# Performance work log

Hardware: AMD Instinct MI355X
Metric: run time of the kernel (lower is better)

Reference implementation:

```python
import jax, jax.numpy as jnp
import numpy as np
import math

B, T, N_EMBD = 8, 4096, 512
DIM = 64  # dim_q == dim_k == dim_v


def setup_inputs() -> dict:
    key = jax.random.key(0)
    k1, k2, k3, k4 = jax.random.split(key, 4)
    x = jax.random.normal(k1, (B, T, N_EMBD), dtype=jnp.float32)
    # store Linear weights as [in, out] so projection is x @ W
    w_q = jax.random.normal(k2, (N_EMBD, DIM), dtype=jnp.float32) * 0.02
    w_k = jax.random.normal(k3, (N_EMBD, DIM), dtype=jnp.float32) * 0.02
    w_v = jax.random.normal(k4, (N_EMBD, DIM), dtype=jnp.float32) * 0.02
    return {"x": x, "w_q": w_q, "w_k": w_k, "w_v": w_v}


def reference(x, w_q, w_k, w_v):
    # Faithful to original torch code, INCLUDING the bug v = w_k(x).
    q = jnp.einsum('btn,nd->btd', x, w_q)
    k = jnp.einsum('btn,nd->btd', x, w_k)
    v = jnp.einsum('btn,nd->btd', x, w_k)  # original uses w_k for v (bug preserved)
    scores = jnp.einsum('bqd,bkd->bqk', q, k) / math.sqrt(DIM)  # [B,T,T]
    causal = jnp.tril(jnp.ones((T, T), dtype=bool))
    scores = jnp.where(causal, scores, jnp.float32(-jnp.inf))
    attn = jax.nn.softmax(scores, axis=-1)
    out = jnp.einsum('bqk,bkd->bqd', attn, v)
    return out
```

## Files before the change

kernel.cpp:

```cpp
#include <hip/hip_runtime.h>
#include <math.h>

#define BB 8
#define TT 4096
#define NE 512
#define DD 64

using f32x4 = __attribute__((ext_vector_type(4))) float;
using s16x8 = __attribute__((ext_vector_type(8))) short;

#define EXP2 __builtin_amdgcn_exp2f

__device__ __forceinline__ ushort f2bf(float f) {
  uint u = __builtin_bit_cast(uint, f);
  u += 0x7fffu + ((u >> 16) & 1u);
  return (ushort)(u >> 16);
}
__device__ __forceinline__ uint cvtpk(float lo, float hi) {
  uint r;
  asm("v_cvt_pk_bf16_f32 %0, %1, %2" : "=v"(r) : "v"(lo), "v"(hi));
  return r;
}

#define KTSWZ(d) ((((d) ^ ((d) >> 3)) & 7) << 4)

__global__ __launch_bounds__(256) void prep_kernel(
    const float* __restrict__ wq, const float* __restrict__ wk,
    ushort* __restrict__ WT) {
  const int i = blockIdx.x * 256 + threadIdx.x;
  const int col = i & 127, k = i >> 7;
  const float v = (col < DD) ? wq[(size_t)k * DD + col] * 0.18033688f
                             : wk[(size_t)k * DD + (col - DD)];
  WT[(size_t)col * NE + k] = f2bf(v);
}

__global__ __launch_bounds__(256) void proj_kernel(
    const float* __restrict__ x, const ushort* __restrict__ WT,
    ushort* __restrict__ Qo, ushort* __restrict__ Ko) {
  __shared__ __align__(16) char smem[24576];
  char* As = smem;
  char* Bs = smem + 8192;
  const int t = threadIdx.x;
  const int w = t >> 6, l = t & 63;
  const int lm = l & 15, lg = l >> 4;
  const int wr = w >> 1, wc = w & 1;
  const size_t rbase = (size_t)blockIdx.x * 64;

  const int arow = t >> 2, akq = (t & 3) * 16;
  const int bcol = t >> 1, bkh = (t & 1) * 32;

  f32x4 acc[2][4];
#pragma unroll
  for (int mt = 0; mt < 2; ++mt)
#pragma unroll
    for (int nt = 0; nt < 4; ++nt) acc[mt][nt] = (f32x4)0.f;

  float4 xa0, xa1, xa2, xa3;
  uint4 wb0, wb1, wb2, wb3;
  {
    const float* xp = x + (rbase + arow) * NE + akq;
    xa0 = *(const float4*)(xp + 0);  xa1 = *(const float4*)(xp + 4);
    xa2 = *(const float4*)(xp + 8);  xa3 = *(const float4*)(xp + 12);
    const ushort* wp = WT + (size_t)bcol * NE + bkh;
    wb0 = *(const uint4*)(wp + 0);   wb1 = *(const uint4*)(wp + 8);
    wb2 = *(const uint4*)(wp + 16);  wb3 = *(const uint4*)(wp + 24);
  }

  for (int kstep = 0; kstep < NE; kstep += 64) {
    __syncthreads();
    {
      uint4 a0, a1;
      a0.x = cvtpk(xa0.x, xa0.y); a0.y = cvtpk(xa0.z, xa0.w);
      a0.z = cvtpk(xa1.x, xa1.y); a0.w = cvtpk(xa1.z, xa1.w);
      a1.x = cvtpk(xa2.x, xa2.y); a1.y = cvtpk(xa2.z, xa2.w);
      a1.z = cvtpk(xa3.x, xa3.y); a1.w = cvtpk(xa3.z, xa3.w);
      const int swa = (arow & 7) << 4;
      *(uint4*)(As + arow * 128 + ((akq * 2) ^ swa)) = a0;
      *(uint4*)(As + arow * 128 + ((akq * 2 + 16) ^ swa)) = a1;
      const int swb = (bcol & 7) << 4;
      *(uint4*)(Bs + bcol * 128 + ((bkh * 2) ^ swb)) = wb0;
      *(uint4*)(Bs + bcol * 128 + ((bkh * 2 + 16) ^ swb)) = wb1;
      *(uint4*)(Bs + bcol * 128 + ((bkh * 2 + 32) ^ swb)) = wb2;
      *(uint4*)(Bs + bcol * 128 + ((bkh * 2 + 48) ^ swb)) = wb3;
    }
    __syncthreads();
    {
      const int kn = (kstep + 64 < NE) ? kstep + 64 : kstep;
      const float* xp = x + (rbase + arow) * NE + kn + akq;
      xa0 = *(const float4*)(xp + 0);  xa1 = *(const float4*)(xp + 4);
      xa2 = *(const float4*)(xp + 8);  xa3 = *(const float4*)(xp + 12);
      const ushort* wp = WT + (size_t)bcol * NE + kn + bkh;
      wb0 = *(const uint4*)(wp + 0);   wb1 = *(const uint4*)(wp + 8);
      wb2 = *(const uint4*)(wp + 16);  wb3 = *(const uint4*)(wp + 24);
    }
#pragma unroll
    for (int ks = 0; ks < 2; ++ks) {
      s16x8 af[2];
#pragma unroll
      for (int mt = 0; mt < 2; ++mt) {
        const int row = wr * 32 + mt * 16 + lm;
        af[mt] = *(const s16x8*)(As + row * 128 + ((ks * 64 + lg * 16) ^ ((row & 7) << 4)));
      }
#pragma unroll
      for (int nt = 0; nt < 4; ++nt) {
        const int col = wc * 64 + nt * 16 + lm;
        s16x8 bf = *(const s16x8*)(Bs + col * 128 + ((ks * 64 + lg * 16) ^ ((col & 7) << 4)));
#pragma unroll
        for (int mt = 0; mt < 2; ++mt)
          acc[mt][nt] = __builtin_amdgcn_mfma_f32_16x16x32_bf16(af[mt], bf, acc[mt][nt], 0, 0, 0);
      }
    }
  }
#pragma unroll
  for (int nt = 0; nt < 4; ++nt) {
    const int col = wc * 64 + nt * 16 + lm;
    ushort* dst = (col < DD) ? Qo : Ko;
    const int c = col & 63;
#pragma unroll
    for (int mt = 0; mt < 2; ++mt)
#pragma unroll
      for (int r = 0; r < 4; ++r) {
        const size_t row = rbase + wr * 32 + mt * 16 + 4 * lg + r;
        dst[row * DD + c] = f2bf(acc[mt][nt][r]);
      }
  }
}

__global__ __launch_bounds__(256) void attn_kernel(
    const ushort* __restrict__ Qg, const ushort* __restrict__ Kg,
    float* __restrict__ PO, float* __restrict__ ML, float* __restrict__ Od,
    int S) {
  __shared__ __align__(16) char smem[32768];
  char* Kl  = smem;
  char* KTl = smem + 8192;
  char* Pl  = smem + 16384;

  const int t = threadIdx.x;
  const int w = t >> 6, l = t & 63;
  const int lm = l & 15, lg = l >> 4;
  int idx = blockIdx.x;
  const int s = idx % S; idx /= S;
  const int pr = idx & 15;
  const int b = idx >> 4;
  const size_t bbase = (size_t)b * TT;
  char* Pw = Pl + w * 4096;

  const int rp = t >> 3;
  const int dblk = t & 7;
  const int r0 = 2 * rp, r1 = r0 + 1;
  char* const pKl0 = Kl + r0 * 128 + ((dblk * 16) ^ ((r0 & 7) << 4));
  char* const pKl1 = Kl + r1 * 128 + ((dblk * 16) ^ ((r1 & 7) << 4));
  char* pKT[8];
#pragma unroll
  for (int j = 0; j < 8; ++j) {
    const int d = dblk * 8 + j;
    pKT[j] = KTl + d * 128 + ((rp * 4) ^ KTSWZ(d));
  }

  for (int pass = 0; pass < 2; ++pass) {
    const int tile = pass ? (31 - pr) : pr;
    const int qwb = tile * 128 + w * 32;
    const int nc = 2 * tile + 2;
    const int c0 = (s * nc) / S, c1 = ((s + 1) * nc) / S;

    s16x8 qf[2][2];
#pragma unroll
    for (int qi = 0; qi < 2; ++qi)
#pragma unroll
      for (int ks = 0; ks < 2; ++ks)
        qf[qi][ks] = *(const s16x8*)(Qg + (bbase + qwb + qi * 16 + lm) * DD + ks * 32 + lg * 8);

    float mrun[2] = {-1e30f, -1e30f};
    float lrun[2] = {0.f, 0.f};
    f32x4 oacc[2][4];
#pragma unroll
    for (int qi = 0; qi < 2; ++qi)
#pragma unroll
      for (int dt = 0; dt < 4; ++dt) oacc[qi][dt] = (f32x4)0.f;

    uint4 ra, rb;
    {
      const int cc = (c0 < nc) ? c0 : nc - 1;
      const ushort* src = Kg + (bbase + cc * 64 + 2 * rp) * DD + dblk * 8;
      ra = *(const uint4*)src;
      rb = *(const uint4*)(src + DD);
    }

    for (int c = c0; c < c1; ++c) {
      const int kb = c * 64;
      __syncthreads();
      {
        *(uint4*)pKl0 = ra;
        *(uint4*)pKl1 = rb;
        const uint wa[4] = {ra.x, ra.y, ra.z, ra.w};
        const uint wb[4] = {rb.x, rb.y, rb.z, rb.w};
#pragma unroll
        for (int jw = 0; jw < 4; ++jw) {
          const uint lo = (wa[jw] & 0xFFFFu) | (wb[jw] << 16);
          const uint hi = (wa[jw] >> 16) | (wb[jw] & 0xFFFF0000u);
          *(uint*)pKT[2 * jw]     = lo;
          *(uint*)pKT[2 * jw + 1] = hi;
        }
      }
      __syncthreads();
      {
        const int cn = (c + 1 < c1) ? (c + 1) : (nc - 1);
        const ushort* src = Kg + (bbase + cn * 64 + 2 * rp) * DD + dblk * 8;
        ra = *(const uint4*)src;
        rb = *(const uint4*)(src + DD);
      }

      const bool act0 = (kb <= qwb + 15);
      const bool act1 = (kb <= qwb + 31);
      if (!act1) continue;

      f32x4 sa[2][4];
#pragma unroll
      for (int qi = 0; qi < 2; ++qi)
#pragma unroll
        for (int kt = 0; kt < 4; ++kt) sa[qi][kt] = (f32x4)0.f;
      __builtin_amdgcn_s_setprio(1);
#pragma unroll
      for (int ks = 0; ks < 2; ++ks) {
#pragma unroll
        for (int kt = 0; kt < 4; ++kt) {
          const int key = kt * 16 + lm;
          s16x8 af = *(const s16x8*)(Kl + key * 128 + ((ks * 64 + lg * 16) ^ ((key & 7) << 4)));
          if (act0)
            sa[0][kt] = __builtin_amdgcn_mfma_f32_16x16x32_bf16(af, qf[0][ks], sa[0][kt], 0, 0, 0);
          sa[1][kt] = __builtin_amdgcn_mfma_f32_16x16x32_bf16(af, qf[1][ks], sa[1][kt], 0, 0, 0);
        }
      }
      __builtin_amdgcn_s_setprio(0);

#pragma unroll
      for (int qi = 0; qi < 2; ++qi) {
        const bool act = qi ? act1 : act0;
        if (!act) continue;
        const int qg = qwb + qi * 16 + lm;
        if (kb + 63 > qwb + qi * 16) {
#pragma unroll
          for (int kt = 0; kt < 4; ++kt) {
            const int key0 = kb + kt * 16 + 4 * lg;
#pragma unroll
            for (int r = 0; r < 4; ++r)
              if (key0 + r > qg) sa[qi][kt][r] = -1e30f;
          }
        }
        float mc = -1e30f;
#pragma unroll
        for (int kt = 0; kt < 4; ++kt)
#pragma unroll
          for (int r = 0; r < 4; ++r) mc = fmaxf(mc, sa[qi][kt][r]);
        mc = fmaxf(mc, __shfl_xor(mc, 16));
        mc = fmaxf(mc, __shfl_xor(mc, 32));
        if (__any(mc > mrun[qi] + 8.f)) {
          const float mn = fmaxf(mrun[qi], mc);
          const float corr = EXP2(mrun[qi] - mn);
          lrun[qi] *= corr;
#pragma unroll
          for (int dt = 0; dt < 4; ++dt) oacc[qi][dt] *= corr;
          mrun[qi] = mn;
        }
        const float mn = mrun[qi];
        float ps = 0.f;
        char* const Pq = Pw + (qi * 16 + lm) * 128;
        const int swp = (lm & 7) << 4;
#pragma unroll
        for (int kt = 0; kt < 4; ++kt) {
          float pv[4];
#pragma unroll
          for (int r = 0; r < 4; ++r) {
            pv[r] = EXP2(sa[qi][kt][r] - mn);
            ps += pv[r];
          }
          const int off = kt * 32 + lg * 8;
          *(uint*)(Pq + (off ^ swp))       = cvtpk(pv[0], pv[1]);
          *(uint*)(Pq + ((off + 4) ^ swp)) = cvtpk(pv[2], pv[3]);
        }
        ps += __shfl_xor(ps, 16);
        ps += __shfl_xor(ps, 32);
        lrun[qi] += ps;
      }

#pragma unroll
      for (int ks = 0; ks < 2; ++ks) {
        s16x8 pf0 = {}, pf1 = {};
        if (act0) pf0 = *(const s16x8*)(Pw + lm * 128 + ((ks * 64 + lg * 16) ^ ((lm & 7) << 4)));
        if (act1) pf1 = *(const s16x8*)(Pw + (16 + lm) * 128 + ((ks * 64 + lg * 16) ^ ((lm & 7) << 4)));
        __builtin_amdgcn_s_setprio(1);
#pragma unroll
        for (int dt = 0; dt < 4; ++dt) {
          const int d = dt * 16 + lm;
          s16x8 vf = *(const s16x8*)(KTl + d * 128 + ((ks * 64 + lg * 16) ^ KTSWZ(d)));
          if (act0) oacc[0][dt] = __builtin_amdgcn_mfma_f32_16x16x32_bf16(vf, pf0, oacc[0][dt], 0, 0, 0);
          if (act1) oacc[1][dt] = __builtin_amdgcn_mfma_f32_16x16x32_bf16(vf, pf1, oacc[1][dt], 0, 0, 0);
        }
        __builtin_amdgcn_s_setprio(0);
      }
    }

    if (S == 1) {
#pragma unroll
      for (int qi = 0; qi < 2; ++qi) {
        const size_t qrow = bbase + qwb + qi * 16 + lm;
        const float inv = 1.f / lrun[qi];
#pragma unroll
        for (int dt = 0; dt < 4; ++dt) {
          f32x4 v = oacc[qi][dt] * inv;
          *(f32x4*)(Od + qrow * DD + dt * 16 + 4 * lg) = v;
        }
      }
    } else {
#pragma unroll
      for (int qi = 0; qi < 2; ++qi) {
        const size_t prow = ((size_t)s * BB + b) * TT + qwb + qi * 16 + lm;
#pragma unroll
        for (int dt = 0; dt < 4; ++dt)
          *(f32x4*)(PO + prow * DD + dt * 16 + 4 * lg) = oacc[qi][dt];
        if (lg == 0) {
          ML[prow * 2] = mrun[qi];
          ML[prow * 2 + 1] = lrun[qi];
        }
      }
    }
  }
}

__global__ __launch_bounds__(256) void merge_kernel(
    const float* __restrict__ PO, const float* __restrict__ ML,
    float* __restrict__ O, int S) {
  const int flat = blockIdx.x * 256 + threadIdx.x;
  const int q = flat >> 4;
  const int d0 = (flat & 15) * 4;
  float mt = -1e30f;
  for (int s = 0; s < S; ++s)
    mt = fmaxf(mt, ML[((size_t)s * BB * TT + q) * 2]);
  float lsum = 0.f;
  f32x4 acc = (f32x4)0.f;
  for (int s = 0; s < S; ++s) {
    const size_t prow = (size_t)s * BB * TT + q;
    const float m = ML[prow * 2], lv = ML[prow * 2 + 1];
    const float wgt = EXP2(m - mt);
    lsum = fmaf(wgt, lv, lsum);
    const f32x4 po = *(const f32x4*)(PO + prow * DD + d0);
#pragma unroll
    for (int i = 0; i < 4; ++i) acc[i] = fmaf(wgt, po[i], acc[i]);
  }
  const float inv = 1.f / lsum;
#pragma unroll
  for (int i = 0; i < 4; ++i) acc[i] *= inv;
  *(f32x4*)(O + (size_t)q * DD + d0) = acc;
}

extern "C" void kernel_launch(void* const* d_in, const int* in_sizes, int n_in,
                              void* d_out, int out_size, void* d_ws, size_t ws_size,
                              hipStream_t stream) {
  const float* x  = (const float*)d_in[0];
  const float* wq = (const float*)d_in[1];
  const float* wk = (const float*)d_in[2];
  float* out = (float*)d_out;

  const size_t rows = (size_t)BB * TT;
  ushort* WT   = (ushort*)d_ws;
  ushort* Qbuf = WT + (size_t)128 * NE;
  ushort* Kbuf = Qbuf + rows * DD;
  char*  after = (char*)(Kbuf + rows * DD);
  const size_t used = (size_t)(after - (char*)d_ws);
  const size_t per  = rows * 2 * 4 + rows * DD * 4;
  int S = 1;
  if (used + 8 * per <= ws_size) S = 8;
  else if (used + 4 * per <= ws_size) S = 4;
  else if (used + 2 * per <= ws_size) S = 2;
  float* ML = (float*)after;
  float* PO = ML + (size_t)S * rows * 2;

  prep_kernel<<<dim3(256), dim3(256), 0, stream>>>(wq, wk, WT);
  proj_kernel<<<dim3(512), dim3(256), 0, stream>>>(x, WT, Qbuf, Kbuf);
  attn_kernel<<<dim3(BB * 16 * S), dim3(256), 0, stream>>>(Qbuf, Kbuf, PO, ML, out, S);
  if (S > 1)
    merge_kernel<<<dim3(2048), dim3(256), 0, stream>>>(PO, ML, out, S);
}
```

Measured before the change: 88.08 us.

## Use variable split-K per tile, register P via permlane swaps, smaller LDS

The fixed S-way split with paired tiles is replaced by a triangular grid in which each query tile is split into a number of KV segments proportional to its causal length (k = tile/4 + 1). This is meant to balance per-block work. The softmax probabilities now stay in registers and are rearranged into MFMA operand layout with v_permlane32/16_swap instead of a round-trip through shared memory. That halves LDS to 16KB and allows a 4-blocks-per-SM launch bound. The merge kernel now only processes rows past the first 512, which have more than one split. The workspace is assumed to hold 8 splits without checking its size.

```diff
diff --git a/kernel.cpp b/kernel.cpp
--- a/kernel.cpp
+++ b/kernel.cpp
@@ -20,6 +20,12 @@
   uint r;
   asm("v_cvt_pk_bf16_f32 %0, %1, %2" : "=v"(r) : "v"(lo), "v"(hi));
   return r;
+}
+__device__ __forceinline__ void pl32swap(uint& a, uint& b) {
+  asm("v_permlane32_swap_b32 %0, %1" : "+v"(a), "+v"(b));
+}
+__device__ __forceinline__ void pl16swap(uint& a, uint& b) {
+  asm("v_permlane16_swap_b32 %0, %1" : "+v"(a), "+v"(b));
 }
 
 #define KTSWZ(d) ((((d) ^ ((d) >> 3)) & 7) << 4)
@@ -126,24 +132,31 @@
   }
 }
 
-__global__ __launch_bounds__(256) void attn_kernel(
+__global__ __launch_bounds__(256, 4) void attn_kernel(
     const ushort* __restrict__ Qg, const ushort* __restrict__ Kg,
-    float* __restrict__ PO, float* __restrict__ ML, float* __restrict__ Od,
-    int S) {
-  __shared__ __align__(16) char smem[32768];
+    float* __restrict__ PO, float* __restrict__ ML, float* __restrict__ Od) {
+  __shared__ __align__(16) char smem[16384];
   char* Kl  = smem;
   char* KTl = smem + 8192;
-  char* Pl  = smem + 16384;
 
   const int t = threadIdx.x;
   const int w = t >> 6, l = t & 63;
   const int lm = l & 15, lg = l >> 4;
-  int idx = blockIdx.x;
-  const int s = idx % S; idx /= S;
-  const int pr = idx & 15;
-  const int b = idx >> 4;
+
+  const int bid = blockIdx.x;
+  const int b = bid / 144;
+  const int id2 = bid - b * 144;
+  int k = 1;
+  while (k < 8 && id2 >= 2 * k * (k + 1)) ++k;
+  const int r_ = id2 - 2 * k * (k - 1);
+  const int tq_ = r_ / k;
+  const int tile = 4 * (k - 1) + tq_;
+  const int s = r_ - tq_ * k;
+  const int nc = 2 * tile + 2;
+  const int c0 = (s * nc) / k, c1 = ((s + 1) * nc) / k;
+
   const size_t bbase = (size_t)b * TT;
-  char* Pw = Pl + w * 4096;
+  const int qwb = tile * 128 + w * 32;
 
   const int rp = t >> 3;
   const int dblk = t & 7;
@@ -157,171 +170,166 @@
     pKT[j] = KTl + d * 128 + ((rp * 4) ^ KTSWZ(d));
   }
 
-  for (int pass = 0; pass < 2; ++pass) {
-    const int tile = pass ? (31 - pr) : pr;
-    const int qwb = tile * 128 + w * 32;
-    const int nc = 2 * tile + 2;
-    const int c0 = (s * nc) / S, c1 = ((s + 1) * nc) / S;
-
-    s16x8 qf[2][2];
-#pragma unroll
-    for (int qi = 0; qi < 2; ++qi)
-#pragma unroll
-      for (int ks = 0; ks < 2; ++ks)
-        qf[qi][ks] = *(const s16x8*)(Qg + (bbase + qwb + qi * 16 + lm) * DD + ks * 32 + lg * 8);
-
-    float mrun[2] = {-1e30f, -1e30f};
-    float lrun[2] = {0.f, 0.f};
-    f32x4 oacc[2][4];
-#pragma unroll
-    for (int qi = 0; qi < 2; ++qi)
-#pragma unroll
-      for (int dt = 0; dt < 4; ++dt) oacc[qi][dt] = (f32x4)0.f;
-
-    uint4 ra, rb;
+  s16x8 qf[2][2];
+#pragma unroll
+  for (int qi = 0; qi < 2; ++qi)
+#pragma unroll
+    for (int ks = 0; ks < 2; ++ks)
+      qf[qi][ks] = *(const s16x8*)(Qg + (bbase + qwb + qi * 16 + lm) * DD + ks * 32 + lg * 8);
+
+  float mrun[2] = {-1e30f, -1e30f};
+  float lrun[2] = {0.f, 0.f};
+  f32x4 oacc[2][4];
+#pragma unroll
+  for (int qi = 0; qi < 2; ++qi)
+#pragma unroll
+    for (int dt = 0; dt < 4; ++dt) oacc[qi][dt] = (f32x4)0.f;
+
+  uint4 ra, rb;
+  {
+    const ushort* src = Kg + (bbase + c0 * 64 + r0) * DD + dblk * 8;
+    ra = *(const uint4*)src;
+    rb = *(const uint4*)(src + DD);
+  }
+
+  for (int c = c0; c < c1; ++c) {
+    const int kb = c * 64;
+    __syncthreads();
     {
-      const int cc = (c0 < nc) ? c0 : nc - 1;
-      const ushort* src = Kg + (bbase + cc * 64 + 2 * rp) * DD + dblk * 8;
+      *(uint4*)pKl0 = ra;
+      *(uint4*)pKl1 = rb;
+      const uint wa[4] = {ra.x, ra.y, ra.z, ra.w};
+      const uint wb[4] = {rb.x, rb.y, rb.z, rb.w};
+#pragma unroll
+      for (int jw = 0; jw < 4; ++jw) {
+        const uint lo = (wa[jw] & 0xFFFFu) | (wb[jw] << 16);
+        const uint hi = (wa[jw] >> 16) | (wb[jw] & 0xFFFF0000u);
+        *(uint*)pKT[2 * jw]     = lo;
+        *(uint*)pKT[2 * jw + 1] = hi;
+      }
+    }
+    __syncthreads();
+    {
+      const int cn = (c + 1 < c1) ? (c + 1) : (nc - 1);
+      const ushort* src = Kg + (bbase + cn * 64 + r0) * DD + dblk * 8;
       ra = *(const uint4*)src;
       rb = *(const uint4*)(src + DD);
     }
 
-    for (int c = c0; c < c1; ++c) {
-      const int kb = c * 64;
-      __syncthreads();
-      {
-        *(uint4*)pKl0 = ra;
-        *(uint4*)pKl1 = rb;
-        const uint wa[4] = {ra.x, ra.y, ra.z, ra.w};
-        const uint wb[4] = {rb.x, rb.y, rb.z, rb.w};
-#pragma unroll
-        for (int jw = 0; jw < 4; ++jw) {
-          const uint lo = (wa[jw] & 0xFFFFu) | (wb[jw] << 16);
-          const uint hi = (wa[jw] >> 16) | (wb[jw] & 0xFFFF0000u);
-          *(uint*)pKT[2 * jw]     = lo;
-          *(uint*)pKT[2 * jw + 1] = hi;
+    if (kb > qwb + 31) continue;
+
+    f32x4 sa[2][4];
+#pragma unroll
+    for (int qi = 0; qi < 2; ++qi)
+#pragma unroll
+      for (int kt = 0; kt < 4; ++kt) sa[qi][kt] = (f32x4)0.f;
+    __builtin_amdgcn_s_setprio(1);
+#pragma unroll
+    for (int ks = 0; ks < 2; ++ks) {
+#pragma unroll
+      for (int kt = 0; kt < 4; ++kt) {
+        const int key = kt * 16 + lm;
+        s16x8 af = *(const s16x8*)(Kl + key * 128 + ((ks * 64 + lg * 16) ^ ((key & 7) << 4)));
+        sa[0][kt] = __builtin_amdgcn_mfma_f32_16x16x32_bf16(af, qf[0][ks], sa[0][kt], 0, 0, 0);
+        sa[1][kt] = __builtin_amdgcn_mfma_f32_16x16x32_bf16(af, qf[1][ks], sa[1][kt], 0, 0, 0);
+      }
+    }
+    __builtin_amdgcn_s_setprio(0);
+
+    uint fragP[2][2][4];
+#pragma unroll
+    for (int qi = 0; qi < 2; ++qi) {
+      const int qg = qwb + qi * 16 + lm;
+      if (kb + 63 > qwb + qi * 16) {
+#pragma unroll
+        for (int kt = 0; kt < 4; ++kt) {
+          const int key0 = kb + kt * 16 + 4 * lg;
+#pragma unroll
+          for (int r = 0; r < 4; ++r)
+            if (key0 + r > qg) sa[qi][kt][r] = -1e30f;
         }
       }
-      __syncthreads();
-      {
-        const int cn = (c + 1 < c1) ? (c + 1) : (nc - 1);
-        const ushort* src = Kg + (bbase + cn * 64 + 2 * rp) * DD + dblk * 8;
-        ra = *(const uint4*)src;
-        rb = *(const uint4*)(src + DD);
-      }
-
-      const bool act0 = (kb <= qwb + 15);
-      const bool act1 = (kb <= qwb + 31);
-      if (!act1) continue;
-
-      f32x4 sa[2][4];
-#pragma unroll
-      for (int qi = 0; qi < 2; ++qi)
-#pragma unroll
-        for (int kt = 0; kt < 4; ++kt) sa[qi][kt] = (f32x4)0.f;
-      __builtin_amdgcn_s_setprio(1);
+      float mc = -1e30f;
+#pragma unroll
+      for (int kt = 0; kt < 4; ++kt)
+#pragma unroll
+        for (int r = 0; r < 4; ++r) mc = fmaxf(mc, sa[qi][kt][r]);
+      mc = fmaxf(mc, __shfl_xor(mc, 16));
+      mc = fmaxf(mc, __shfl_xor(mc, 32));
+      if (__any(mc > mrun[qi] + 8.f)) {
+        const float mn = fmaxf(mrun[qi], mc);
+        const float corr = EXP2(mrun[qi] - mn);
+        lrun[qi] *= corr;
+#pragma unroll
+        for (int dt = 0; dt < 4; ++dt) oacc[qi][dt] *= corr;
+        mrun[qi] = mn;
+      }
+      const float mn = mrun[qi];
+      float ps = 0.f;
+      uint pk[4][2];
+#pragma unroll
+      for (int kt = 0; kt < 4; ++kt) {
+        float pv[4];
+#pragma unroll
+        for (int r = 0; r < 4; ++r) {
+          pv[r] = EXP2(sa[qi][kt][r] - mn);
+          ps += pv[r];
+        }
+        pk[kt][0] = cvtpk(pv[0], pv[1]);
+        pk[kt][1] = cvtpk(pv[2], pv[3]);
+      }
+      ps += __shfl_xor(ps, 16);
+      ps += __shfl_xor(ps, 32);
+      lrun[qi] += ps;
 #pragma unroll
       for (int ks = 0; ks < 2; ++ks) {
-#pragma unroll
-        for (int kt = 0; kt < 4; ++kt) {
-          const int key = kt * 16 + lm;
-          s16x8 af = *(const s16x8*)(Kl + key * 128 + ((ks * 64 + lg * 16) ^ ((key & 7) << 4)));
-          if (act0)
-            sa[0][kt] = __builtin_amdgcn_mfma_f32_16x16x32_bf16(af, qf[0][ks], sa[0][kt], 0, 0, 0);
-          sa[1][kt] = __builtin_amdgcn_mfma_f32_16x16x32_bf16(af, qf[1][ks], sa[1][kt], 0, 0, 0);
-        }
-      }
-      __builtin_amdgcn_s_setprio(0);
-
-#pragma unroll
-      for (int qi = 0; qi < 2; ++qi) {
-        const bool act = qi ? act1 : act0;
-        if (!act) continue;
-        const int qg = qwb + qi * 16 + lm;
-        if (kb + 63 > qwb + qi * 16) {
-#pragma unroll
-          for (int kt = 0; kt < 4; ++kt) {
-            const int key0 = kb + kt * 16 + 4 * lg;
-#pragma unroll
-            for (int r = 0; r < 4; ++r)
-              if (key0 + r > qg) sa[qi][kt][r] = -1e30f;
-          }
-        }
-        float mc = -1e30f;
-#pragma unroll
-        for (int kt = 0; kt < 4; ++kt)
-#pragma unroll
-          for (int r = 0; r < 4; ++r) mc = fmaxf(mc, sa[qi][kt][r]);
-        mc = fmaxf(mc, __shfl_xor(mc, 16));
-        mc = fmaxf(mc, __shfl_xor(mc, 32));
-        if (__any(mc > mrun[qi] + 8.f)) {
-          const float mn = fmaxf(mrun[qi], mc);
-          const float corr = EXP2(mrun[qi] - mn);
-          lrun[qi] *= corr;
-#pragma unroll
-          for (int dt = 0; dt < 4; ++dt) oacc[qi][dt] *= corr;
-          mrun[qi] = mn;
-        }
-        const float mn = mrun[qi];
-        float ps = 0.f;
-        char* const Pq = Pw + (qi * 16 + lm) * 128;
-        const int swp = (lm & 7) << 4;
-#pragma unroll
-        for (int kt = 0; kt < 4; ++kt) {
-          float pv[4];
-#pragma unroll
-          for (int r = 0; r < 4; ++r) {
-            pv[r] = EXP2(sa[qi][kt][r] - mn);
-            ps += pv[r];
-          }
-          const int off = kt * 32 + lg * 8;
-          *(uint*)(Pq + (off ^ swp))       = cvtpk(pv[0], pv[1]);
-          *(uint*)(Pq + ((off + 4) ^ swp)) = cvtpk(pv[2], pv[3]);
-        }
-        ps += __shfl_xor(ps, 16);
-        ps += __shfl_xor(ps, 32);
-        lrun[qi] += ps;
-      }
-
-#pragma unroll
-      for (int ks = 0; ks < 2; ++ks) {
-        s16x8 pf0 = {}, pf1 = {};
-        if (act0) pf0 = *(const s16x8*)(Pw + lm * 128 + ((ks * 64 + lg * 16) ^ ((lm & 7) << 4)));
-        if (act1) pf1 = *(const s16x8*)(Pw + (16 + lm) * 128 + ((ks * 64 + lg * 16) ^ ((lm & 7) << 4)));
-        __builtin_amdgcn_s_setprio(1);
-#pragma unroll
-        for (int dt = 0; dt < 4; ++dt) {
-          const int d = dt * 16 + lm;
-          s16x8 vf = *(const s16x8*)(KTl + d * 128 + ((ks * 64 + lg * 16) ^ KTSWZ(d)));
-          if (act0) oacc[0][dt] = __builtin_amdgcn_mfma_f32_16x16x32_bf16(vf, pf0, oacc[0][dt], 0, 0, 0);
-          if (act1) oacc[1][dt] = __builtin_amdgcn_mfma_f32_16x16x32_bf16(vf, pf1, oacc[1][dt], 0, 0, 0);
-        }
-        __builtin_amdgcn_s_setprio(0);
-      }
-    }
-
-    if (S == 1) {
-#pragma unroll
-      for (int qi = 0; qi < 2; ++qi) {
-        const size_t qrow = bbase + qwb + qi * 16 + lm;
-        const float inv = 1.f / lrun[qi];
-#pragma unroll
-        for (int dt = 0; dt < 4; ++dt) {
-          f32x4 v = oacc[qi][dt] * inv;
-          *(f32x4*)(Od + qrow * DD + dt * 16 + 4 * lg) = v;
-        }
-      }
-    } else {
-#pragma unroll
-      for (int qi = 0; qi < 2; ++qi) {
-        const size_t prow = ((size_t)s * BB + b) * TT + qwb + qi * 16 + lm;
-#pragma unroll
-        for (int dt = 0; dt < 4; ++dt)
-          *(f32x4*)(PO + prow * DD + dt * 16 + 4 * lg) = oacc[qi][dt];
-        if (lg == 0) {
-          ML[prow * 2] = mrun[qi];
-          ML[prow * 2 + 1] = lrun[qi];
-        }
+        uint R0 = pk[2 * ks][0], R1 = pk[2 * ks][1];
+        uint R2 = pk[2 * ks + 1][0], R3 = pk[2 * ks + 1][1];
+        pl32swap(R0, R2); pl32swap(R1, R3);
+        pl16swap(R0, R2); pl16swap(R1, R3);
+        fragP[qi][ks][0] = R0; fragP[qi][ks][1] = R1;
+        fragP[qi][ks][2] = R2; fragP[qi][ks][3] = R3;
+      }
+    }
+
+    __builtin_amdgcn_s_setprio(1);
+#pragma unroll
+    for (int ks = 0; ks < 2; ++ks) {
+      union { uint u[4]; s16x8 v; } p0, p1;
+#pragma unroll
+      for (int j = 0; j < 4; ++j) { p0.u[j] = fragP[0][ks][j]; p1.u[j] = fragP[1][ks][j]; }
+#pragma unroll
+      for (int dt = 0; dt < 4; ++dt) {
+        const int d = dt * 16 + lm;
+        s16x8 vf = *(const s16x8*)(KTl + d * 128 + ((ks * 64 + lg * 16) ^ KTSWZ(d)));
+        oacc[0][dt] = __builtin_amdgcn_mfma_f32_16x16x32_bf16(vf, p0.v, oacc[0][dt], 0, 0, 0);
+        oacc[1][dt] = __builtin_amdgcn_mfma_f32_16x16x32_bf16(vf, p1.v, oacc[1][dt], 0, 0, 0);
+      }
+    }
+    __builtin_amdgcn_s_setprio(0);
+  }
+
+  if (k == 1) {
+#pragma unroll
+    for (int qi = 0; qi < 2; ++qi) {
+      const size_t qrow = bbase + qwb + qi * 16 + lm;
+      const float inv = 1.f / lrun[qi];
+#pragma unroll
+      for (int dt = 0; dt < 4; ++dt) {
+        f32x4 v = oacc[qi][dt] * inv;
+        *(f32x4*)(Od + qrow * DD + dt * 16 + 4 * lg) = v;
+      }
+    }
+  } else {
+#pragma unroll
+    for (int qi = 0; qi < 2; ++qi) {
+      const size_t prow = ((size_t)s * BB + b) * TT + qwb + qi * 16 + lm;
+#pragma unroll
+      for (int dt = 0; dt < 4; ++dt)
+        *(f32x4*)(PO + prow * DD + dt * 16 + 4 * lg) = oacc[qi][dt];
+      if (lg == 0) {
+        ML[prow * 2] = mrun[qi];
+        ML[prow * 2 + 1] = lrun[qi];
       }
     }
   }
@@ -329,17 +337,20 @@
 
 __global__ __launch_bounds__(256) void merge_kernel(
     const float* __restrict__ PO, const float* __restrict__ ML,
-    float* __restrict__ O, int S) {
+    float* __restrict__ O) {
   const int flat = blockIdx.x * 256 + threadIdx.x;
-  const int q = flat >> 4;
+  const int qo = flat >> 4;
   const int d0 = (flat & 15) * 4;
+  const int b = qo / 3584;
+  const int qrow = 512 + (qo - b * 3584);
+  const int St = (qrow >> 9) + 1;
   float mt = -1e30f;
-  for (int s = 0; s < S; ++s)
-    mt = fmaxf(mt, ML[((size_t)s * BB * TT + q) * 2]);
+  for (int s = 0; s < St; ++s)
+    mt = fmaxf(mt, ML[(((size_t)s * BB + b) * TT + qrow) * 2]);
   float lsum = 0.f;
   f32x4 acc = (f32x4)0.f;
-  for (int s = 0; s < S; ++s) {
-    const size_t prow = (size_t)s * BB * TT + q;
+  for (int s = 0; s < St; ++s) {
+    const size_t prow = ((size_t)s * BB + b) * TT + qrow;
     const float m = ML[prow * 2], lv = ML[prow * 2 + 1];
     const float wgt = EXP2(m - mt);
     lsum = fmaf(wgt, lv, lsum);
@@ -350,7 +361,7 @@
   const float inv = 1.f / lsum;
 #pragma unroll
   for (int i = 0; i < 4; ++i) acc[i] *= inv;
-  *(f32x4*)(O + (size_t)q * DD + d0) = acc;
+  *(f32x4*)(O + ((size_t)b * TT + qrow) * DD + d0) = acc;
 }
 
 extern "C" void kernel_launch(void* const* d_in, const int* in_sizes, int n_in,
@@ -365,19 +376,11 @@
   ushort* WT   = (ushort*)d_ws;
   ushort* Qbuf = WT + (size_t)128 * NE;
   ushort* Kbuf = Qbuf + rows * DD;
-  char*  after = (char*)(Kbuf + rows * DD);
-  const size_t used = (size_t)(after - (char*)d_ws);
-  const size_t per  = rows * 2 * 4 + rows * DD * 4;
-  int S = 1;
-  if (used + 8 * per <= ws_size) S = 8;
-  else if (used + 4 * per <= ws_size) S = 4;
-  else if (used + 2 * per <= ws_size) S = 2;
-  float* ML = (float*)after;
-  float* PO = ML + (size_t)S * rows * 2;
+  float* ML = (float*)(Kbuf + rows * DD);
+  float* PO = ML + (size_t)8 * rows * 2;
 
   prep_kernel<<<dim3(256), dim3(256), 0, stream>>>(wq, wk, WT);
   proj_kernel<<<dim3(512), dim3(256), 0, stream>>>(x, WT, Qbuf, Kbuf);
-  attn_kernel<<<dim3(BB * 16 * S), dim3(256), 0, stream>>>(Qbuf, Kbuf, PO, ML, out, S);
-  if (S > 1)
-    merge_kernel<<<dim3(2048), dim3(256), 0, stream>>>(PO, ML, out, S);
-}
+  attn_kernel<<<dim3(BB * 144), dim3(256), 0, stream>>>(Qbuf, Kbuf, PO, ML, out);
+  merge_kernel<<<dim3(1792), dim3(256), 0, stream>>>(PO, ML, out);
+}
```

Result: faster. 83.46 us (-5.2%).
